# Performance work log

Hardware: AMD Instinct MI355X
Metric: run time of the kernel (lower is better)

Reference implementation:

```python
import jax, jax.numpy as jnp
import numpy as np

ALPHA = 0.99
EPS = 1e-14


def setup_inputs() -> dict:
    key = jax.random.key(0)
    B, C, T, F = 16, 1, 2000, 481
    x = jax.random.normal(key, (B, C, T, F, 2), dtype=jnp.float32)
    # unit_norm_init: linearly decaying initial norm state over freq bins
    init_state = jnp.linspace(0.001, 0.0001, F, dtype=jnp.float32).reshape(1, 1, F, 1)
    return {"x": x, "init_state": init_state}


def reference(x, init_state):
    # x: [B, C, T, F, 2] (real/imag), init_state: [1, 1, F, 1]
    B, C, T, F, _ = x.shape
    # complex magnitude per (b,c,t,f), clamped for stability: [B, C, T, F, 1]
    x_abs = jnp.sqrt(jnp.maximum(jnp.sum(x * x, axis=-1, keepdims=True), EPS))
    # scan over time: state = (1-alpha)*|x_t| + alpha*state
    xs = jnp.moveaxis(x_abs, 2, 0)  # [T, B, C, F, 1]
    s0 = jnp.broadcast_to(init_state, (B, C, F, 1)).astype(x.dtype)

    def step(s, xt):
        s = xt * (1.0 - ALPHA) + s * ALPHA
        return s, s

    _, states = jax.lax.scan(step, s0, xs)  # [T, B, C, F, 1]
    states = jnp.moveaxis(states, 0, 2)  # [B, C, T, F, 1]
    return x / jnp.sqrt(states)
```

## Files before the change

### kernel.cpp

```cpp
#include <hip/hip_runtime.h>


#define ALPHA_F 0.99f
#define OMA_F   0.01f
#define EPS_F   1e-14f

constexpr int Bn = 16;
constexpr int Tn = 2000;
constexpr int Fn = 481;
constexpr int NC = 100;
constexpr int L  = Tn / NC;
constexpr int MT = 25;
#define ALPHA_L 0.817906938f

__global__ __launch_bounds__(256) void eun_pass1(
    const float* __restrict__ x, float* __restrict__ part) {
  const int f = blockIdx.x * blockDim.x + threadIdx.x;
  if (f >= Fn) return;
  const int b = blockIdx.y;
  const int c = blockIdx.z;

  const size_t stride = (size_t)Fn * 2;
  const float* xp = x + ((size_t)b * Tn + (size_t)c * L) * stride + (size_t)f * 2;

  float2 v[L];
#pragma unroll
  for (int j = 0; j < L; ++j)
    v[j] = *(const float2*)(xp + (size_t)j * stride);

  float s = 0.f;
#pragma unroll
  for (int j = 0; j < L; ++j) {
    float m = sqrtf(fmaxf(fmaf(v[j].x, v[j].x, v[j].y * v[j].y), EPS_F));
    s = fmaf(ALPHA_F, s, OMA_F * m);
  }
  part[((size_t)b * NC + c) * Fn + f] = s;
}

__global__ __launch_bounds__(256) void eun_mid(
    const float* __restrict__ init_state, float* __restrict__ part) {
  const int f = blockIdx.x * blockDim.x + threadIdx.x;
  if (f >= Fn) return;
  const int b = blockIdx.y;

  float* pp = part + (size_t)b * NC * Fn + f;
  float s = init_state[f];
  for (int c0 = 0; c0 < NC; c0 += MT) {
    float p[MT];
#pragma unroll
    for (int k = 0; k < MT; ++k) p[k] = pp[(size_t)(c0 + k) * Fn];
#pragma unroll
    for (int k = 0; k < MT; ++k) {
      pp[(size_t)(c0 + k) * Fn] = s;
      s = fmaf(s, ALPHA_L, p[k]);
    }
  }
}

__global__ __launch_bounds__(256) void eun_pass2(
    const float* __restrict__ x, const float* __restrict__ start,
    float* __restrict__ out) {
  const int f = blockIdx.x * blockDim.x + threadIdx.x;
  if (f >= Fn) return;
  const int b = blockIdx.y;
  const int c = blockIdx.z;

  float s = start[((size_t)b * NC + c) * Fn + f];

  const size_t stride = (size_t)Fn * 2;
  const size_t off = ((size_t)b * Tn + (size_t)c * L) * stride + (size_t)f * 2;
  const float* xp = x + off;
  float*       op = out + off;

  float2 v[L];
#pragma unroll
  for (int j = 0; j < L; ++j)
    v[j] = *(const float2*)(xp + (size_t)j * stride);

#pragma unroll
  for (int j = 0; j < L; ++j) {
    float m = sqrtf(fmaxf(fmaf(v[j].x, v[j].x, v[j].y * v[j].y), EPS_F));
    s = fmaf(ALPHA_F, s, OMA_F * m);
    float inv = rsqrtf(s);
    union { float2 f2; unsigned long long u; } cvt;
    cvt.f2 = make_float2(v[j].x * inv, v[j].y * inv);
    __builtin_nontemporal_store(cvt.u,
        (unsigned long long*)(op + (size_t)j * stride));
  }
}

extern "C" void kernel_launch(void* const* d_in, const int* in_sizes, int n_in,
                              void* d_out, int out_size, void* d_ws, size_t ws_size,
                              hipStream_t stream) {
  const float* x    = (const float*)d_in[0];
  const float* init = (const float*)d_in[1];
  float* out        = (float*)d_out;
  float* part       = (float*)d_ws;

  dim3 grid3((Fn + 255) / 256, Bn, NC);
  eun_pass1<<<grid3, dim3(256), 0, stream>>>(x, part);
  eun_mid<<<dim3((Fn + 255) / 256, Bn), dim3(256), 0, stream>>>(init, part);
  eun_pass2<<<grid3, dim3(256), 0, stream>>>(x, part, out);
}
```

Baseline: 239.4 us.

## Stage time-slabs through LDS for coalesced 16-byte loads and stores

Both passes now have each block own one (batch, chunk) pair across all frequencies, with every thread handling two frequency bins. Pass1 loads 4-row slabs as coalesced float4 into double-buffered LDS and prefetches the next slab during the scan. Pass2 prefetches per-thread float2 inputs, writes the normalized results into LDS, then emits coalesced float4 nontemporal stores. The aim is to replace strided 8-byte accesses with full-width contiguous transactions, at the cost of fewer blocks (1600 instead of 3200), block-wide barriers and LDS traffic.

```diff
diff --git a/kernel.cpp b/kernel.cpp
--- a/kernel.cpp
+++ b/kernel.cpp
@@ -5,36 +5,72 @@
 #define OMA_F   0.01f
 #define EPS_F   1e-14f
 
+typedef float f32x4 __attribute__((ext_vector_type(4)));
+
 constexpr int Bn = 16;
 constexpr int Tn = 2000;
 constexpr int Fn = 481;
 constexpr int NC = 100;
 constexpr int L  = Tn / NC;
+constexpr int ST = 4;
+constexpr int NST = L / ST;
+constexpr int RF  = 2 * Fn;
+constexpr int SF4 = ST * RF / 4;
+constexpr int TL3 = SF4 - 3 * 256;
 constexpr int MT = 25;
 #define ALPHA_L 0.817906938f
 
 __global__ __launch_bounds__(256) void eun_pass1(
     const float* __restrict__ x, float* __restrict__ part) {
-  const int f = blockIdx.x * blockDim.x + threadIdx.x;
-  if (f >= Fn) return;
-  const int b = blockIdx.y;
-  const int c = blockIdx.z;
+  __shared__ f32x4 lds[2][SF4];
+  const int tid = threadIdx.x;
+  const int c = blockIdx.x, b = blockIdx.y;
 
-  const size_t stride = (size_t)Fn * 2;
-  const float* xp = x + ((size_t)b * Tn + (size_t)c * L) * stride + (size_t)f * 2;
+  const size_t base_f = ((size_t)b * Tn + (size_t)c * L) * RF;
+  const f32x4* xb = (const f32x4*)(x + base_f);
 
-  float2 v[L];
+  f32x4 v[4];
 #pragma unroll
-  for (int j = 0; j < L; ++j)
-    v[j] = *(const float2*)(xp + (size_t)j * stride);
+  for (int j = 0; j < 3; ++j) v[j] = xb[tid + 256 * j];
+  if (tid < TL3) v[3] = xb[tid + 256 * 3];
+#pragma unroll
+  for (int j = 0; j < 3; ++j) lds[0][tid + 256 * j] = v[j];
+  if (tid < TL3) lds[0][tid + 256 * 3] = v[3];
+  __syncthreads();
 
-  float s = 0.f;
+  const int f1 = tid, f2 = tid + 256;
+  float s1 = 0.f, s2 = 0.f;
+  int cur = 0;
+  for (int st = 0; st < NST; ++st) {
+    if (st + 1 < NST) {
+      const f32x4* sb = xb + (size_t)(st + 1) * SF4;
 #pragma unroll
-  for (int j = 0; j < L; ++j) {
-    float m = sqrtf(fmaxf(fmaf(v[j].x, v[j].x, v[j].y * v[j].y), EPS_F));
-    s = fmaf(ALPHA_F, s, OMA_F * m);
+      for (int j = 0; j < 3; ++j) v[j] = sb[tid + 256 * j];
+      if (tid < TL3) v[3] = sb[tid + 256 * 3];
+    }
+    const float2* l2 = (const float2*)lds[cur];
+#pragma unroll
+    for (int r = 0; r < ST; ++r) {
+      float2 a = l2[r * Fn + f1];
+      float m = sqrtf(fmaxf(fmaf(a.x, a.x, a.y * a.y), EPS_F));
+      s1 = fmaf(ALPHA_F, s1, OMA_F * m);
+      if (f2 < Fn) {
+        float2 q = l2[r * Fn + f2];
+        float m2 = sqrtf(fmaxf(fmaf(q.x, q.x, q.y * q.y), EPS_F));
+        s2 = fmaf(ALPHA_F, s2, OMA_F * m2);
+      }
+    }
+    if (st + 1 < NST) {
+#pragma unroll
+      for (int j = 0; j < 3; ++j) lds[cur ^ 1][tid + 256 * j] = v[j];
+      if (tid < TL3) lds[cur ^ 1][tid + 256 * 3] = v[3];
+    }
+    __syncthreads();
+    cur ^= 1;
   }
-  part[((size_t)b * NC + c) * Fn + f] = s;
+  float* pp = part + ((size_t)b * NC + c) * Fn;
+  pp[f1] = s1;
+  if (f2 < Fn) pp[f2] = s2;
 }
 
 __global__ __launch_bounds__(256) void eun_mid(
@@ -42,7 +78,6 @@
   const int f = blockIdx.x * blockDim.x + threadIdx.x;
   if (f >= Fn) return;
   const int b = blockIdx.y;
-
   float* pp = part + (size_t)b * NC * Fn + f;
   float s = init_state[f];
   for (int c0 = 0; c0 < NC; c0 += MT) {
@@ -60,32 +95,67 @@
 __global__ __launch_bounds__(256) void eun_pass2(
     const float* __restrict__ x, const float* __restrict__ start,
     float* __restrict__ out) {
-  const int f = blockIdx.x * blockDim.x + threadIdx.x;
-  if (f >= Fn) return;
-  const int b = blockIdx.y;
-  const int c = blockIdx.z;
+  __shared__ f32x4 lds[2][SF4];
+  const int tid = threadIdx.x;
+  const int c = blockIdx.x, b = blockIdx.y;
 
-  float s = start[((size_t)b * NC + c) * Fn + f];
+  const size_t base_f = ((size_t)b * Tn + (size_t)c * L) * RF;
+  const int f1 = tid, f2 = tid + 256;
+  const bool a2 = (f2 < Fn);
 
-  const size_t stride = (size_t)Fn * 2;
-  const size_t off = ((size_t)b * Tn + (size_t)c * L) * stride + (size_t)f * 2;
-  const float* xp = x + off;
-  float*       op = out + off;
+  float s1 = start[((size_t)b * NC + c) * Fn + f1];
+  float s2 = a2 ? start[((size_t)b * NC + c) * Fn + f2] : 0.f;
 
-  float2 v[L];
+  const float* xp1 = x + base_f + (size_t)f1 * 2;
+  const float* xp2 = x + base_f + (size_t)f2 * 2;
+
+  float2 av[ST], qv[ST], an[ST], qn[ST];
 #pragma unroll
-  for (int j = 0; j < L; ++j)
-    v[j] = *(const float2*)(xp + (size_t)j * stride);
+  for (int r = 0; r < ST; ++r) {
+    av[r] = *(const float2*)(xp1 + (size_t)r * RF);
+    if (a2) qv[r] = *(const float2*)(xp2 + (size_t)r * RF);
+  }
 
+  int cur = 0;
+  for (int st = 0; st < NST; ++st) {
+    if (st + 1 < NST) {
+      const float* p1 = xp1 + (size_t)(st + 1) * ST * RF;
+      const float* p2 = xp2 + (size_t)(st + 1) * ST * RF;
 #pragma unroll
-  for (int j = 0; j < L; ++j) {
-    float m = sqrtf(fmaxf(fmaf(v[j].x, v[j].x, v[j].y * v[j].y), EPS_F));
-    s = fmaf(ALPHA_F, s, OMA_F * m);
-    float inv = rsqrtf(s);
-    union { float2 f2; unsigned long long u; } cvt;
-    cvt.f2 = make_float2(v[j].x * inv, v[j].y * inv);
-    __builtin_nontemporal_store(cvt.u,
-        (unsigned long long*)(op + (size_t)j * stride));
+      for (int r = 0; r < ST; ++r) {
+        an[r] = *(const float2*)(p1 + (size_t)r * RF);
+        if (a2) qn[r] = *(const float2*)(p2 + (size_t)r * RF);
+      }
+    }
+    float2* l2 = (float2*)lds[cur];
+#pragma unroll
+    for (int r = 0; r < ST; ++r) {
+      float m = sqrtf(fmaxf(fmaf(av[r].x, av[r].x, av[r].y * av[r].y), EPS_F));
+      s1 = fmaf(ALPHA_F, s1, OMA_F * m);
+      float inv1 = rsqrtf(s1);
+      l2[r * Fn + f1] = make_float2(av[r].x * inv1, av[r].y * inv1);
+      if (a2) {
+        float m2 = sqrtf(fmaxf(fmaf(qv[r].x, qv[r].x, qv[r].y * qv[r].y), EPS_F));
+        s2 = fmaf(ALPHA_F, s2, OMA_F * m2);
+        float inv2 = rsqrtf(s2);
+        l2[r * Fn + f2] = make_float2(qv[r].x * inv2, qv[r].y * inv2);
+      }
+    }
+    __syncthreads();
+    f32x4* ob = (f32x4*)(out + base_f) + (size_t)st * SF4;
+    const f32x4* ls = (const f32x4*)lds[cur];
+#pragma unroll
+    for (int j = 0; j < 3; ++j) {
+      f32x4 o = ls[tid + 256 * j];
+      __builtin_nontemporal_store(o, ob + tid + 256 * j);
+    }
+    if (tid < TL3) {
+      f32x4 o = ls[tid + 256 * 3];
+      __builtin_nontemporal_store(o, ob + tid + 256 * 3);
+    }
+#pragma unroll
+    for (int r = 0; r < ST; ++r) { av[r] = an[r]; qv[r] = qn[r]; }
+    cur ^= 1;
   }
 }
 
@@ -97,8 +167,8 @@
   float* out        = (float*)d_out;
   float* part       = (float*)d_ws;
 
-  dim3 grid3((Fn + 255) / 256, Bn, NC);
-  eun_pass1<<<grid3, dim3(256), 0, stream>>>(x, part);
+  dim3 grid(NC, Bn);
+  eun_pass1<<<grid, dim3(256), 0, stream>>>(x, part);
   eun_mid<<<dim3((Fn + 255) / 256, Bn), dim3(256), 0, stream>>>(init, part);
-  eun_pass2<<<grid3, dim3(256), 0, stream>>>(x, part, out);
+  eun_pass2<<<grid, dim3(256), 0, stream>>>(x, part, out);
 }
```

Measured after the change: 241.6 us. No clear change (+0.9%).
